# Kernel tuning notes

Measured on AMD Instinct MI355X. Metric: run time of the kernel, lower is better.

The kernel has to match this reference:

```python
import jax, jax.numpy as jnp
import numpy as np

QLEN, MLEN, BSZ = 1024, 1024, 2
D_MODEL, H, D_HEAD, D_FF = 1024, 16, 64, 4096
KLEN = QLEN + MLEN


def _ln(x, g, b, eps=1e-5):
    mu = jnp.mean(x, axis=-1, keepdims=True)
    var = jnp.var(x, axis=-1, keepdims=True)
    return (x - mu) * jax.lax.rsqrt(var + eps) * g + b


def _rel_shift(x):
    # x: [q, k, b, n] -> Transformer-XL relative shift
    q, k, b, n = x.shape
    zp = jnp.zeros((q, 1, b, n), x.dtype)
    xp = jnp.concatenate([zp, x], axis=1).reshape(k + 1, q, b, n)[1:]
    return xp.reshape(q, k, b, n)


def setup_inputs() -> dict:
    key = jax.random.key(0)
    ks = jax.random.split(key, 12)
    s = 0.02
    inp = {
        "input_": jax.random.normal(ks[0], (QLEN, BSZ, D_MODEL), jnp.float32),
        "mems": jax.random.normal(ks[1], (MLEN, BSZ, D_MODEL), jnp.float32),
        "pos_emb": jax.random.normal(ks[2], (KLEN, 1, D_MODEL), jnp.float32),
        # True = masked. Causal with memory: query i sees keys j <= i + MLEN
        "mask_tgt": jnp.triu(jnp.ones((QLEN, KLEN), bool), k=MLEN + 1),
        "ln1_g": jnp.ones((D_MODEL,), jnp.float32),
        "ln1_b": jnp.zeros((D_MODEL,), jnp.float32),
        "qkv_w": jax.random.normal(ks[3], (D_MODEL, 3 * H * D_HEAD), jnp.float32) * s,
        "qkv_b": jnp.zeros((3 * H * D_HEAD,), jnp.float32),
        "r_w": jax.random.normal(ks[4], (D_MODEL, H * D_HEAD), jnp.float32) * s,
        "r_w_bias": jax.random.normal(ks[5], (H, D_HEAD), jnp.float32) * s,
        "r_r_bias": jax.random.normal(ks[6], (H, D_HEAD), jnp.float32) * s,
        "o_w": jax.random.normal(ks[7], (H * D_HEAD, D_MODEL), jnp.float32) * s,
        "ln2_g": jnp.ones((D_MODEL,), jnp.float32),
        "ln2_b": jnp.zeros((D_MODEL,), jnp.float32),
        "ff_w1": jax.random.normal(ks[8], (D_MODEL, D_FF), jnp.float32) * s,
        "ff_b1": jnp.zeros((D_FF,), jnp.float32),
        "ff_w2": jax.random.normal(ks[9], (D_FF, D_MODEL), jnp.float32) * s,
        "ff_b2": jnp.zeros((D_MODEL,), jnp.float32),
    }
    return inp


def reference(input_, mems, pos_emb, mask_tgt, ln1_g, ln1_b, qkv_w, qkv_b,
              r_w, r_w_bias, r_r_bias, o_w, ln2_g, ln2_b,
              ff_w1, ff_b1, ff_w2, ff_b2):
    qlen, bsz, _ = input_.shape
    # --- pre-norm (applied to both current input and mems) ---
    q_in = _ln(input_, ln1_g, ln1_b)
    m_in = _ln(mems, ln1_g, ln1_b)
    cat = jnp.concatenate([m_in, q_in], axis=0)            # [klen, b, d]
    klen = cat.shape[0]
    heads = cat @ qkv_w + qkv_b                            # [klen, b, 3*h*dh]
    w_q, w_k, w_v = jnp.split(heads, 3, axis=-1)
    w_q = w_q[-qlen:].reshape(qlen, bsz, H, D_HEAD)        # [q, b, h, dh]
    w_k = w_k.reshape(klen, bsz, H, D_HEAD)
    w_v = w_v.reshape(klen, bsz, H, D_HEAD)
    r_k = (pos_emb[:, 0] @ r_w).reshape(klen, H, D_HEAD)   # [k, h, dh]

    AC = jnp.einsum('ibnd,jbnd->ijbn', w_q + r_w_bias, w_k)
    BD = jnp.einsum('ibnd,jnd->ijbn', w_q + r_r_bias, r_k)
    BD = _rel_shift(BD)
    scale = 1.0 / np.sqrt(D_HEAD)
    score = (AC + BD) * scale                              # [q, k, b, h]
    score = jnp.where(mask_tgt[:, :, None, None], -1e30, score)
    prob = jax.nn.softmax(score, axis=1)
    attn = jnp.einsum('ijbn,jbnd->ibnd', prob, w_v).reshape(qlen, bsz, H * D_HEAD)
    attn_out = attn @ o_w                                  # [q, b, d]
    x = input_ + attn_out                                  # residual (dropout = eval)

    # --- FFN block ---
    y = _ln(x, ln2_g, ln2_b)
    y = jax.nn.relu(y @ ff_w1 + ff_b1) @ ff_w2 + ff_b2
    return x + y
```

## Files before the change

kernel.cpp:

```cpp
#include <hip/hip_runtime.h>


typedef unsigned short u16;
typedef unsigned int   u32;
typedef __attribute__((ext_vector_type(8))) short bf16x8;
typedef __attribute__((ext_vector_type(4))) float f32x4;

struct alignas(16) U128 { u32 x[4]; };
struct alignas(16) F128 { float f[4]; };
struct alignas(8)  U64  { u32 x[2]; };

#define DEV static __device__ __forceinline__
#define MF(a, b, c) __builtin_amdgcn_mfma_f32_16x16x32_bf16((a), (b), (c), 0, 0, 0)

typedef __attribute__((address_space(1))) u32 as1_u32;
typedef __attribute__((address_space(3))) u32 as3_u32;
DEV void gload16(const void* g, void* l) {
  __builtin_amdgcn_global_load_lds((as1_u32*)g, (as3_u32*)l, 16, 0, 0);
}

DEV u16 f2bf(float f) {
  union { float f; u32 u; } v; v.f = f;
  u32 r = v.u + 0x7fffu + ((v.u >> 16) & 1u);
  return (u16)(r >> 16);
}
DEV float bf2f(u16 h) {
  union { u32 u; float f; } v; v.u = ((u32)h) << 16;
  return v.f;
}

template <int TWO>
__global__ __launch_bounds__(256) void ln_rows(
    const float* __restrict__ src, const float* __restrict__ src2,
    const float* __restrict__ g, const float* __restrict__ b,
    u16* __restrict__ dst)
{
  int row = blockIdx.x, tid = threadIdx.x;
  const float* s_;
  if constexpr (TWO) s_ = (row < 2048) ? src + (size_t)row * 1024
                                       : src2 + (size_t)(row - 2048) * 1024;
  else s_ = src + (size_t)row * 1024;
  F128 v = ((const F128*)s_)[tid];
  float s = v.f[0] + v.f[1] + v.f[2] + v.f[3];
  float q = v.f[0]*v.f[0] + v.f[1]*v.f[1] + v.f[2]*v.f[2] + v.f[3]*v.f[3];
#pragma unroll
  for (int off = 1; off < 64; off <<= 1) {
    s += __shfl_xor(s, off); q += __shfl_xor(q, off);
  }
  __shared__ float sh[8];
  int wid = tid >> 6;
  if ((tid & 63) == 0) { sh[wid] = s; sh[4 + wid] = q; }
  __syncthreads();
  s = sh[0] + sh[1] + sh[2] + sh[3];
  q = sh[4] + sh[5] + sh[6] + sh[7];
  float mu = s * (1.0f / 1024.0f);
  float rs = rsqrtf(q * (1.0f / 1024.0f) - mu * mu + 1e-5f);
  F128 g4 = ((const F128*)g)[tid];
  F128 b4 = ((const F128*)b)[tid];
  union { u16 h[4]; U64 u; } o;
#pragma unroll
  for (int j = 0; j < 4; j++)
    o.h[j] = f2bf((v.f[j] - mu) * rs * g4.f[j] + b4.f[j]);
  *(U64*)(dst + (size_t)row * 1024 + tid * 4) = o.u;
}

__global__ __launch_bounds__(256) void ln_fuse(
    const u16* __restrict__ p0, const u16* __restrict__ p1,
    const u16* __restrict__ p2, const u16* __restrict__ p3,
    const float* __restrict__ resid, const float* __restrict__ g,
    const float* __restrict__ b, float* __restrict__ X, u16* __restrict__ YN)
{
  int row = blockIdx.x, tid = threadIdx.x;
  U64 a = ((const U64*)(p0 + (size_t)row * 1024))[tid];
  U64 c = ((const U64*)(p1 + (size_t)row * 1024))[tid];
  U64 d = ((const U64*)(p2 + (size_t)row * 1024))[tid];
  U64 e = ((const U64*)(p3 + (size_t)row * 1024))[tid];
  F128 rv = ((const F128*)(resid + (size_t)row * 1024))[tid];
  float x[4];
#pragma unroll
  for (int k = 0; k < 2; k++) {
    x[2*k]   = bf2f((u16)a.x[k]) + bf2f((u16)c.x[k]) + bf2f((u16)d.x[k]) + bf2f((u16)e.x[k]) + rv.f[2*k];
    x[2*k+1] = bf2f((u16)(a.x[k] >> 16)) + bf2f((u16)(c.x[k] >> 16)) + bf2f((u16)(d.x[k] >> 16)) + bf2f((u16)(e.x[k] >> 16)) + rv.f[2*k+1];
  }
  F128 xo;
#pragma unroll
  for (int j = 0; j < 4; j++) xo.f[j] = x[j];
  *(F128*)(X + (size_t)row * 1024 + tid * 4) = xo;

  float s = x[0] + x[1] + x[2] + x[3];
  float q = x[0]*x[0] + x[1]*x[1] + x[2]*x[2] + x[3]*x[3];
#pragma unroll
  for (int off = 1; off < 64; off <<= 1) {
    s += __shfl_xor(s, off); q += __shfl_xor(q, off);
  }
  __shared__ float sh[8];
  int wid = tid >> 6;
  if ((tid & 63) == 0) { sh[wid] = s; sh[4 + wid] = q; }
  __syncthreads();
  s = sh[0] + sh[1] + sh[2] + sh[3];
  q = sh[4] + sh[5] + sh[6] + sh[7];
  float mu = s * (1.0f / 1024.0f);
  float rs = rsqrtf(q * (1.0f / 1024.0f) - mu * mu + 1e-5f);
  F128 g4 = ((const F128*)g)[tid];
  F128 b4 = ((const F128*)b)[tid];
  union { u16 h[4]; U64 u; } o;
#pragma unroll
  for (int j = 0; j < 4; j++)
    o.h[j] = f2bf((x[j] - mu) * rs * g4.f[j] + b4.f[j]);
  *(U64*)(YN + (size_t)row * 1024 + tid * 4) = o.u;
}

__global__ __launch_bounds__(256) void prep_weights(
    const float* __restrict__ qkvw, const float* __restrict__ rw,
    const float* __restrict__ oww, const float* __restrict__ fw1,
    const float* __restrict__ fw2, const float* __restrict__ pos,
    u16* __restrict__ WT_QKV, u16* __restrict__ WT_R, u16* __restrict__ WT_O,
    u16* __restrict__ WT_F1, u16* __restrict__ WT_F2, u16* __restrict__ POSB)
{
  int id = blockIdx.x, tid = threadIdx.x;
  if (id >= 3328) {
    int i = (id - 3328) * 256 + tid;
    F128 v = ((const F128*)pos)[i];
    union { u16 h[4]; U64 u; } o;
#pragma unroll
    for (int j = 0; j < 4; j++) o.h[j] = f2bf(v.f[j]);
    ((U64*)POSB)[i] = o.u;
    return;
  }
  const float* W; u16* Wt; int K, N, rem;
  if (id < 768)       { W = qkvw; Wt = WT_QKV; K = 1024; N = 3072; rem = id; }
  else if (id < 1024) { W = rw;   Wt = WT_R;   K = 1024; N = 1024; rem = id - 768; }
  else if (id < 1280) { W = oww;  Wt = WT_O;   K = 1024; N = 1024; rem = id - 1024; }
  else if (id < 2304) { W = fw1;  Wt = WT_F1;  K = 1024; N = 4096; rem = id - 1280; }
  else                { W = fw2;  Wt = WT_F2;  K = 4096; N = 1024; rem = id - 2304; }
  int nn = N >> 6;
  int k0 = (rem / nn) * 64, n0 = (rem % nn) * 64;
  __shared__ float t[64][65];
  int r = tid >> 6, c = tid & 63;
#pragma unroll
  for (int i = 0; i < 16; i++)
    t[r + i * 4][c] = W[(size_t)(k0 + r + i * 4) * N + n0 + c];
  __syncthreads();
#pragma unroll
  for (int i = 0; i < 16; i++) {
    int n = r + i * 4;
    Wt[(size_t)(n0 + n) * K + k0 + c] = f2bf(t[c][n]);
  }
}

template <int EPI, int NSPLIT>
__global__ __launch_bounds__(256, 2) void gemm_bt(
    const u16* __restrict__ A, const u16* __restrict__ Bt,
    u16* __restrict__ outb, const float* __restrict__ bias,
    u16* __restrict__ p0, u16* __restrict__ p1,
    u16* __restrict__ p2, u16* __restrict__ p3,
    int M, int N, int K)
{
  __shared__ u16 As[2][128 * 64];
  __shared__ u16 Bs[2][128 * 64];
  int tid = threadIdx.x;
  int m0 = blockIdx.x * 128, n0 = blockIdx.y * 128;
  int lane = tid & 63, wid = tid >> 6;
  int wr = wid >> 1, wc = wid & 1;
  f32x4 acc[4][4] = {};

  const int Kc = K / NSPLIT;
  const int kbase = (NSPLIT > 1) ? (int)blockIdx.z * Kc : 0;

  const int lrow = wid * 8 + (lane >> 3);
  const int lcol = (lane & 7) * 8;
  const u16* Ag = A  + (size_t)(m0 + lrow) * K + kbase + lcol;
  const u16* Bg = Bt + (size_t)(n0 + lrow) * K + kbase + lcol;

  auto stage = [&](int buf, int k0) {
#pragma unroll
    for (int i = 0; i < 4; i++) {
      gload16(Ag + (size_t)i * 32 * K + k0, &As[buf][(i * 4 + wid) * 512]);
      gload16(Bg + (size_t)i * 32 * K + k0, &Bs[buf][(i * 4 + wid) * 512]);
    }
  };

  stage(0, 0);
  __syncthreads();
  int cur = 0;
  for (int k0 = 0; k0 < Kc; k0 += 64) {
    if (k0 + 64 < Kc) stage(cur ^ 1, k0 + 64);
    bf16x8 af[2][4], bfr[2][4];
#pragma unroll
    for (int kc = 0; kc < 2; kc++)
#pragma unroll
      for (int f = 0; f < 4; f++) {
        af[kc][f]  = *(const bf16x8*)&As[cur][(wr * 64 + f * 16 + (lane & 15)) * 64 + kc * 32 + (lane >> 4) * 8];
        bfr[kc][f] = *(const bf16x8*)&Bs[cur][(wc * 64 + f * 16 + (lane & 15)) * 64 + kc * 32 + (lane >> 4) * 8];
      }
    __builtin_amdgcn_s_setprio(1);
#pragma unroll
    for (int kc = 0; kc < 2; kc++)
#pragma unroll
      for (int fi = 0; fi < 4; fi++)
#pragma unroll
        for (int fj = 0; fj < 4; fj++)
          acc[fi][fj] = MF(af[kc][fi], bfr[kc][fj], acc[fi][fj]);
    __builtin_amdgcn_s_setprio(0);
    __syncthreads();
    cur ^= 1;
  }

  u16* part = nullptr;
  if constexpr (NSPLIT > 1) {
    part = (blockIdx.z == 0) ? p0 : (blockIdx.z == 1) ? p1
         : (blockIdx.z == 2) ? p2 : p3;
  }
#pragma unroll
  for (int fi = 0; fi < 4; fi++)
#pragma unroll
    for (int fj = 0; fj < 4; fj++) {
      int col = n0 + wc * 64 + fj * 16 + (lane & 15);
      float bvv = (NSPLIT == 1 && bias != nullptr) ? bias[col] : 0.0f;
#pragma unroll
      for (int r = 0; r < 4; r++) {
        int row = m0 + wr * 64 + fi * 16 + (lane >> 4) * 4 + r;
        float v = acc[fi][fj][r] + bvv;
        if constexpr (NSPLIT > 1) {
          part[(size_t)row * N + col] = f2bf(v);
        } else {
          if constexpr (EPI == 1) v = fmaxf(v, 0.0f);
          outb[(size_t)row * N + col] = f2bf(v);
        }
      }
    }
}

template <int NS, int EPI>
__global__ __launch_bounds__(256) void reduce_splitb(
    const u16* __restrict__ p0, const u16* __restrict__ p1,
    const u16* __restrict__ p2, const u16* __restrict__ p3,
    const float* __restrict__ bias, const float* __restrict__ resid,
    u16* __restrict__ outb, float* __restrict__ outf, int N)
{
  int e = (blockIdx.x * 256 + threadIdx.x) * 8;
  U128 a = *(const U128*)(p0 + e);
  U128 c = *(const U128*)(p1 + e);
  float v[8];
#pragma unroll
  for (int k = 0; k < 4; k++) {
    v[2*k]   = bf2f((u16)a.x[k]) + bf2f((u16)c.x[k]);
    v[2*k+1] = bf2f((u16)(a.x[k] >> 16)) + bf2f((u16)(c.x[k] >> 16));
  }
  if constexpr (NS == 4) {
    U128 d2 = *(const U128*)(p2 + e);
    U128 d3 = *(const U128*)(p3 + e);
#pragma unroll
    for (int k = 0; k < 4; k++) {
      v[2*k]   += bf2f((u16)d2.x[k]) + bf2f((u16)d3.x[k]);
      v[2*k+1] += bf2f((u16)(d2.x[k] >> 16)) + bf2f((u16)(d3.x[k] >> 16));
    }
  }
  if constexpr (EPI == 2) {
    F128 r0 = *(const F128*)(resid + e);
    F128 r1 = *(const F128*)(resid + e + 4);
    int col = e % N;
    F128 o0, o1;
#pragma unroll
    for (int j = 0; j < 4; j++) {
      float b0 = (bias != nullptr) ? bias[col + j] : 0.0f;
      float b1 = (bias != nullptr) ? bias[col + 4 + j] : 0.0f;
      o0.f[j] = v[j] + b0 + r0.f[j];
      o1.f[j] = v[4 + j] + b1 + r1.f[j];
    }
    *(F128*)(outf + e) = o0;
    *(F128*)(outf + e + 4) = o1;
  } else {
    U128 o;
#pragma unroll
    for (int k = 0; k < 4; k++)
      o.x[k] = (u32)f2bf(v[2*k]) | ((u32)f2bf(v[2*k+1]) << 16);
    *(U128*)(outb + e) = o;
  }
}

__global__ __launch_bounds__(256) void extract_vt(
    const u16* __restrict__ heads, u16* __restrict__ Vt)
{
  __shared__ u16 t[64][72];
  int jt = blockIdx.x;
  int bh = blockIdx.y;
  int b = bh >> 4, h = bh & 15;
  int tid = threadIdx.x;
  int row = tid >> 2;
  int cc = (tid & 3) * 16;
#pragma unroll
  for (int i = 0; i < 2; i++)
    *(U128*)&t[row][cc + i * 8] =
        *(const U128*)&heads[(size_t)((jt * 64 + row) * 2 + b) * 3072 + 2048 + h * 64 + cc + i * 8];
  __syncthreads();
  int jc = tid & 63, dr = tid >> 6;
#pragma unroll
  for (int i = 0; i < 16; i++) {
    int d = dr + i * 4;
    Vt[((size_t)bh * 64 + d) * 2048 + jt * 64 + jc] = t[jc][d];
  }
}

__global__ __launch_bounds__(256, 2) void attn_fwd(
    const u16* __restrict__ heads, const u16* __restrict__ rk,
    const u16* __restrict__ Vt, const float* __restrict__ rwb,
    const float* __restrict__ rrb, u16* __restrict__ attnout)
{
  __shared__ u16 lds[37376];

  int tid = threadIdx.x, lane = tid & 63, wid = tid >> 6;
  int bh = blockIdx.x;
  int y = (int)blockIdx.y;
  int xt = (y < 8) ? y : 23 - y;
  int i0 = xt * 64;
  int b = bh >> 4, h = bh & 15;
  const float SCL = 0.18033688f;

  u16* Ps = lds + 32768;
  u16* Qw = lds;
  u16* Qr = lds + 4608;

  for (int c = tid; c < 512; c += 256) {
    int row = c >> 3, c8 = (c & 7) * 8;
    union { U128 v; u16 h[8]; } in, ow, orr;
    in.v = *(const U128*)&heads[(size_t)((1024 + i0 + row) * 2 + b) * 3072 + h * 64 + c8];
#pragma unroll
    for (int j = 0; j < 8; j++) {
      float q = bf2f(in.h[j]);
      ow.h[j]  = f2bf(q + rwb[h * 64 + c8 + j]);
      orr.h[j] = f2bf(q + rrb[h * 64 + c8 + j]);
    }
    *(U128*)&Qw[row * 72 + c8] = ow.v;
    *(U128*)&Qr[row * 72 + c8] = orr.v;
  }
  __syncthreads();

  bf16x8 qwf[2], qrf[2];
  int qrow = wid * 16 + (lane & 15);
#pragma unroll
  for (int kc = 0; kc < 2; kc++) {
    qwf[kc] = *(const bf16x8*)&Qw[qrow * 72 + kc * 32 + (lane >> 4) * 8];
    qrf[kc] = *(const bf16x8*)&Qr[qrow * 72 + kc * 32 + (lane >> 4) * 8];
  }
  __syncthreads();

  const int srow = lane >> 3;
  const int scol = 8 * ((lane & 7) ^ srow);

  auto stage = [&](int buf, int t) {
    int j0 = t * 64;
    u16* base = lds + buf * 16384;
#pragma unroll
    for (int i = 0; i < 2; i++) {
      int g8 = wid * 2 + i;
      int jr = j0 + g8 * 8 + srow;
      gload16(heads + (size_t)(jr * 2 + b) * 3072 + 1024 + h * 64 + scol,
              base + g8 * 512);
    }
#pragma unroll
    for (int i = 0; i < 2; i++) {
      int g8 = wid * 2 + i;
      int dr = g8 * 8 + srow;
      gload16(Vt + ((size_t)bh * 64 + dr) * 2048 + j0 + scol,
              base + 4096 + g8 * 512);
    }
    int rbase = 960 + j0 - i0;
#pragma unroll
    for (int i = 0; i < 4; i++) {
      int g8 = wid * 4 + i;
      int rr = rbase + g8 * 8 + srow;
      rr = rr < 0 ? 0 : (rr > 2047 ? 2047 : rr);
      gload16(rk + (size_t)rr * 1024 + h * 64 + scol,
              base + 8192 + g8 * 512);
    }
  };

  stage(0, 0);
  __syncthreads();

  float mrow[4], plrow[4];
  f32x4 o[4] = {};
  f32x4 bd[5];
#pragma unroll
  for (int r = 0; r < 4; r++) { mrow[r] = -1e30f; plrow[r] = 0.0f; }

  int nt = i0 / 64 + 17;
  const int roffw = 48 - wid * 16;
  const int g = lane >> 4, cc = lane & 15;
  const int rswz = 8 * (lane & 7);

  for (int t = 0; t < nt; t++) {
    const u16* base = lds + (t & 1) * 16384;
    if (t + 1 < nt) stage((t + 1) & 1, t + 1);

    const u16* Kb = base;
    const u16* Vb = base + 4096;
    const u16* Rb = base + 8192;

    f32x4 sAC[4] = {};
    if (t == 0) bd[0] = (f32x4){0.f, 0.f, 0.f, 0.f};
#pragma unroll
    for (int fb = 1; fb < 5; fb++) bd[fb] = (f32x4){0.f, 0.f, 0.f, 0.f};
    __builtin_amdgcn_s_setprio(1);
#pragma unroll
    for (int kc = 0; kc < 2; kc++) {
      int cb = (kc * 32 + g * 8) ^ rswz;
#pragma unroll
      for (int fj = 0; fj < 4; fj++) {
        bf16x8 kf = *(const bf16x8*)&Kb[(fj * 16 + (lane & 15)) * 64 + cb];
        sAC[fj] = MF(qwf[kc], kf, sAC[fj]);
      }
      if (t == 0) {
        bf16x8 rf = *(const bf16x8*)&Rb[(roffw + (lane & 15)) * 64 + cb];
        bd[0] = MF(qrf[kc], rf, bd[0]);
      }
#pragma unroll
      for (int fb = 1; fb < 5; fb++) {
        bf16x8 rf = *(const bf16x8*)&Rb[(roffw + fb * 16 + (lane & 15)) * 64 + cb];
        bd[fb] = MF(qrf[kc], rf, bd[fb]);
      }
    }
    __builtin_amdgcn_s_setprio(0);

    float p[4][4];
#pragma unroll
    for (int fj = 0; fj < 4; fj++)
#pragma unroll
      for (int r = 0; r < 4; r++) {
        int sh_ = 15 - 4 * g - r;
        int src = (lane & 48) | ((lane + sh_) & 15);
        float lo = __shfl(bd[fj][r], src);
        float hi = __shfl(bd[fj + 1][r], src);
        float bdv = (cc + sh_ < 16) ? lo : hi;
        p[fj][r] = (sAC[fj][r] + bdv) * SCL;
      }
    bd[0] = bd[4];

    if (t == nt - 1) {
#pragma unroll
      for (int fj = 0; fj < 4; fj++)
#pragma unroll
        for (int r = 0; r < 4; r++)
          if (fj * 16 + cc > 16 * wid + 4 * g + r) p[fj][r] = -1e30f;
    }

    float tmax[4];
#pragma unroll
    for (int r = 0; r < 4; r++)
      tmax[r] = fmaxf(fmaxf(p[0][r], p[1][r]), fmaxf(p[2][r], p[3][r]));

    bool ok = true;
#pragma unroll
    for (int r = 0; r < 4; r++) ok &= (tmax[r] <= mrow[r] + 12.0f);
    if (!__all(ok)) {
#pragma unroll
      for (int off = 1; off < 16; off <<= 1)
#pragma unroll
        for (int r = 0; r < 4; r++)
          tmax[r] = fmaxf(tmax[r], __shfl_xor(tmax[r], off));
#pragma unroll
      for (int r = 0; r < 4; r++) {
        float mn = fmaxf(mrow[r], tmax[r]);
        float ms = exp2f(mrow[r] - mn);
        mrow[r] = mn;
        plrow[r] *= ms;
#pragma unroll
        for (int fd = 0; fd < 4; fd++) o[fd][r] *= ms;
      }
    }

#pragma unroll
    for (int fj = 0; fj < 4; fj++)
#pragma unroll
      for (int r = 0; r < 4; r++) {
        float e = exp2f(p[fj][r] - mrow[r]);
        plrow[r] += e;
        Ps[(wid * 16 + (lane >> 4) * 4 + r) * 72 + fj * 16 + (lane & 15)] = f2bf(e);
      }
    __builtin_amdgcn_s_setprio(1);
#pragma unroll
    for (int kc = 0; kc < 2; kc++) {
      bf16x8 pf = *(const bf16x8*)&Ps[(wid * 16 + (lane & 15)) * 72 + kc * 32 + g * 8];
      int cb = (kc * 32 + g * 8) ^ rswz;
#pragma unroll
      for (int fd = 0; fd < 4; fd++) {
        bf16x8 vf = *(const bf16x8*)&Vb[(fd * 16 + (lane & 15)) * 64 + cb];
        o[fd] = MF(pf, vf, o[fd]);
      }
    }
    __builtin_amdgcn_s_setprio(0);

    __syncthreads();
  }

#pragma unroll
  for (int off = 1; off < 16; off <<= 1)
#pragma unroll
    for (int r = 0; r < 4; r++)
      plrow[r] += __shfl_xor(plrow[r], off);
#pragma unroll
  for (int fd = 0; fd < 4; fd++)
#pragma unroll
    for (int r = 0; r < 4; r++) {
      int ii2 = (lane >> 4) * 4 + r;
      int row = (i0 + wid * 16 + ii2) * 2 + b;
      attnout[(size_t)row * 1024 + h * 64 + fd * 16 + (lane & 15)] = f2bf(o[fd][r] / plrow[r]);
    }
}

extern "C" void kernel_launch(void* const* d_in, const int* in_sizes, int n_in,
                              void* d_out, int out_size, void* d_ws, size_t ws_size,
                              hipStream_t stream)
{
  const float* input_ = (const float*)d_in[0];
  const float* mems   = (const float*)d_in[1];
  const float* pos    = (const float*)d_in[2];
  const float* ln1g = (const float*)d_in[4];
  const float* ln1b = (const float*)d_in[5];
  const float* qkvw = (const float*)d_in[6];
  const float* qkvb = (const float*)d_in[7];
  const float* rw   = (const float*)d_in[8];
  const float* rwb  = (const float*)d_in[9];
  const float* rrb  = (const float*)d_in[10];
  const float* ow   = (const float*)d_in[11];
  const float* ln2g = (const float*)d_in[12];
  const float* ln2b = (const float*)d_in[13];
  const float* fw1  = (const float*)d_in[14];
  const float* fb1  = (const float*)d_in[15];
  const float* fw2  = (const float*)d_in[16];
  const float* fb2  = (const float*)d_in[17];
  float* out = (float*)d_out;

  char* w = (char*)d_ws;
  u16* WT_QKV = (u16*)(w + 0);
  u16* WT_R   = (u16*)(w + 6291456);
  u16* WT_O   = (u16*)(w + 8388608);
  u16* WT_F1  = (u16*)(w + 10485760);
  u16* WT_F2  = (u16*)(w + 18874368);
  u16* POSB   = (u16*)(w + 27262976);
  u16* ATTN   = POSB;
  u16* CATLN  = (u16*)(w + 31457280);
  u16* HEADS  = (u16*)(w + 39845888);
  u16* H1     = HEADS;
  float* X    = (float*)(w + 56623104);
  u16* RK     = (u16*)(w + 65011712);
  u16* VT     = (u16*)(w + 69206016);
  u16* YN     = VT;

  u16* RKP0 = (u16*)(w + 31457280);
  u16* RKP1 = (u16*)(w + 35651584);
  u16* RKP2 = (u16*)(w + 69206016);
  u16* RKP3 = (u16*)(w + 73400320);
  u16* OWP0 = (u16*)(w + 39845888);
  u16* OWP1 = (u16*)(w + 44040192);
  u16* OWP2 = (u16*)(w + 48234496);
  u16* OWP3 = (u16*)(w + 52428800);
  u16* F2P0 = (u16*)(w + 0);
  u16* F2P1 = (u16*)(w + 10485760);
  u16* F2P2 = (u16*)(w + 31457280);
  u16* F2P3 = (u16*)(w + 65011712);

  dim3 blk(256);

  prep_weights<<<dim3(5376), blk, 0, stream>>>(
      qkvw, rw, ow, fw1, fw2, pos, WT_QKV, WT_R, WT_O, WT_F1, WT_F2, POSB);

  ln_rows<1><<<dim3(4096), blk, 0, stream>>>(mems, input_, ln1g, ln1b, CATLN);

  gemm_bt<0, 1><<<dim3(32, 24), blk, 0, stream>>>(
      CATLN, WT_QKV, HEADS, qkvb, nullptr, nullptr, nullptr, nullptr, 4096, 3072, 1024);
  gemm_bt<0, 4><<<dim3(16, 8, 4), blk, 0, stream>>>(
      POSB, WT_R, nullptr, nullptr, RKP0, RKP1, RKP2, RKP3, 2048, 1024, 1024);
  reduce_splitb<4, 0><<<dim3(1024), blk, 0, stream>>>(
      RKP0, RKP1, RKP2, RKP3, nullptr, nullptr, RK, nullptr, 1024);

  extract_vt<<<dim3(32, 32), blk, 0, stream>>>(HEADS, VT);
  attn_fwd<<<dim3(32, 16), blk, 0, stream>>>(HEADS, RK, VT, rwb, rrb, ATTN);

  gemm_bt<0, 4><<<dim3(16, 8, 4), blk, 0, stream>>>(
      ATTN, WT_O, nullptr, nullptr, OWP0, OWP1, OWP2, OWP3, 2048, 1024, 1024);
  ln_fuse<<<dim3(2048), blk, 0, stream>>>(
      OWP0, OWP1, OWP2, OWP3, input_, ln2g, ln2b, X, YN);

  gemm_bt<1, 1><<<dim3(16, 32), blk, 0, stream>>>(
      YN, WT_F1, H1, fb1, nullptr, nullptr, nullptr, nullptr, 2048, 4096, 1024);
  gemm_bt<0, 4><<<dim3(16, 8, 4), blk, 0, stream>>>(
      H1, WT_F2, nullptr, nullptr, F2P0, F2P1, F2P2, F2P3, 2048, 1024, 4096);
  reduce_splitb<4, 2><<<dim3(1024), blk, 0, stream>>>(
      F2P0, F2P1, F2P2, F2P3, fb2, X, nullptr, out, 1024);
}
```

Baseline: 223.3 us.

## Fuse LN1 into prep kernel and single-buffer GEMM LDS for higher occupancy

Merges the first layernorm launch into the weight-prep kernel as extra blocks, removing one kernel launch. Separately, the GEMM drops LDS double-buffering, halving shared memory, and raises launch bounds to 4 blocks per CU so latency is hidden by occupancy rather than prefetch. This costs the overlap of global loads with MFMA inside each block, and the higher launch-bounds target may squeeze registers for the 64-float accumulator.

```diff
diff --git a/kernel.cpp b/kernel.cpp
--- a/kernel.cpp
+++ b/kernel.cpp
@@ -29,20 +29,31 @@
   return v.f;
 }
 
-template <int TWO>
-__global__ __launch_bounds__(256) void ln_rows(
-    const float* __restrict__ src, const float* __restrict__ src2,
-    const float* __restrict__ g, const float* __restrict__ b,
-    u16* __restrict__ dst)
+__global__ __launch_bounds__(256) void ln_fuse(
+    const u16* __restrict__ p0, const u16* __restrict__ p1,
+    const u16* __restrict__ p2, const u16* __restrict__ p3,
+    const float* __restrict__ resid, const float* __restrict__ g,
+    const float* __restrict__ b, float* __restrict__ X, u16* __restrict__ YN)
 {
   int row = blockIdx.x, tid = threadIdx.x;
-  const float* s_;
-  if constexpr (TWO) s_ = (row < 2048) ? src + (size_t)row * 1024
-                                       : src2 + (size_t)(row - 2048) * 1024;
-  else s_ = src + (size_t)row * 1024;
-  F128 v = ((const F128*)s_)[tid];
-  float s = v.f[0] + v.f[1] + v.f[2] + v.f[3];
-  float q = v.f[0]*v.f[0] + v.f[1]*v.f[1] + v.f[2]*v.f[2] + v.f[3]*v.f[3];
+  U64 a = ((const U64*)(p0 + (size_t)row * 1024))[tid];
+  U64 c = ((const U64*)(p1 + (size_t)row * 1024))[tid];
+  U64 d = ((const U64*)(p2 + (size_t)row * 1024))[tid];
+  U64 e = ((const U64*)(p3 + (size_t)row * 1024))[tid];
+  F128 rv = ((const F128*)(resid + (size_t)row * 1024))[tid];
+  float x[4];
+#pragma unroll
+  for (int k = 0; k < 2; k++) {
+    x[2*k]   = bf2f((u16)a.x[k]) + bf2f((u16)c.x[k]) + bf2f((u16)d.x[k]) + bf2f((u16)e.x[k]) + rv.f[2*k];
+    x[2*k+1] = bf2f((u16)(a.x[k] >> 16)) + bf2f((u16)(c.x[k] >> 16)) + bf2f((u16)(d.x[k] >> 16)) + bf2f((u16)(e.x[k] >> 16)) + rv.f[2*k+1];
+  }
+  F128 xo;
+#pragma unroll
+  for (int j = 0; j < 4; j++) xo.f[j] = x[j];
+  *(F128*)(X + (size_t)row * 1024 + tid * 4) = xo;
+
+  float s = x[0] + x[1] + x[2] + x[3];
+  float q = x[0]*x[0] + x[1]*x[1] + x[2]*x[2] + x[3]*x[3];
 #pragma unroll
   for (int off = 1; off < 64; off <<= 1) {
     s += __shfl_xor(s, off); q += __shfl_xor(q, off);
@@ -60,52 +71,6 @@
   union { u16 h[4]; U64 u; } o;
 #pragma unroll
   for (int j = 0; j < 4; j++)
-    o.h[j] = f2bf((v.f[j] - mu) * rs * g4.f[j] + b4.f[j]);
-  *(U64*)(dst + (size_t)row * 1024 + tid * 4) = o.u;
-}
-
-__global__ __launch_bounds__(256) void ln_fuse(
-    const u16* __restrict__ p0, const u16* __restrict__ p1,
-    const u16* __restrict__ p2, const u16* __restrict__ p3,
-    const float* __restrict__ resid, const float* __restrict__ g,
-    const float* __restrict__ b, float* __restrict__ X, u16* __restrict__ YN)
-{
-  int row = blockIdx.x, tid = threadIdx.x;
-  U64 a = ((const U64*)(p0 + (size_t)row * 1024))[tid];
-  U64 c = ((const U64*)(p1 + (size_t)row * 1024))[tid];
-  U64 d = ((const U64*)(p2 + (size_t)row * 1024))[tid];
-  U64 e = ((const U64*)(p3 + (size_t)row * 1024))[tid];
-  F128 rv = ((const F128*)(resid + (size_t)row * 1024))[tid];
-  float x[4];
-#pragma unroll
-  for (int k = 0; k < 2; k++) {
-    x[2*k]   = bf2f((u16)a.x[k]) + bf2f((u16)c.x[k]) + bf2f((u16)d.x[k]) + bf2f((u16)e.x[k]) + rv.f[2*k];
-    x[2*k+1] = bf2f((u16)(a.x[k] >> 16)) + bf2f((u16)(c.x[k] >> 16)) + bf2f((u16)(d.x[k] >> 16)) + bf2f((u16)(e.x[k] >> 16)) + rv.f[2*k+1];
-  }
-  F128 xo;
-#pragma unroll
-  for (int j = 0; j < 4; j++) xo.f[j] = x[j];
-  *(F128*)(X + (size_t)row * 1024 + tid * 4) = xo;
-
-  float s = x[0] + x[1] + x[2] + x[3];
-  float q = x[0]*x[0] + x[1]*x[1] + x[2]*x[2] + x[3]*x[3];
-#pragma unroll
-  for (int off = 1; off < 64; off <<= 1) {
-    s += __shfl_xor(s, off); q += __shfl_xor(q, off);
-  }
-  __shared__ float sh[8];
-  int wid = tid >> 6;
-  if ((tid & 63) == 0) { sh[wid] = s; sh[4 + wid] = q; }
-  __syncthreads();
-  s = sh[0] + sh[1] + sh[2] + sh[3];
-  q = sh[4] + sh[5] + sh[6] + sh[7];
-  float mu = s * (1.0f / 1024.0f);
-  float rs = rsqrtf(q * (1.0f / 1024.0f) - mu * mu + 1e-5f);
-  F128 g4 = ((const F128*)g)[tid];
-  F128 b4 = ((const F128*)b)[tid];
-  union { u16 h[4]; U64 u; } o;
-#pragma unroll
-  for (int j = 0; j < 4; j++)
     o.h[j] = f2bf((x[j] - mu) * rs * g4.f[j] + b4.f[j]);
   *(U64*)(YN + (size_t)row * 1024 + tid * 4) = o.u;
 }
@@ -114,10 +79,41 @@
     const float* __restrict__ qkvw, const float* __restrict__ rw,
     const float* __restrict__ oww, const float* __restrict__ fw1,
     const float* __restrict__ fw2, const float* __restrict__ pos,
+    const float* __restrict__ mems, const float* __restrict__ input_,
+    const float* __restrict__ ln1g, const float* __restrict__ ln1b,
     u16* __restrict__ WT_QKV, u16* __restrict__ WT_R, u16* __restrict__ WT_O,
-    u16* __restrict__ WT_F1, u16* __restrict__ WT_F2, u16* __restrict__ POSB)
+    u16* __restrict__ WT_F1, u16* __restrict__ WT_F2, u16* __restrict__ POSB,
+    u16* __restrict__ CATLN)
 {
   int id = blockIdx.x, tid = threadIdx.x;
+  if (id >= 5376) {
+    int row = id - 5376;
+    const float* s_ = (row < 2048) ? mems + (size_t)row * 1024
+                                   : input_ + (size_t)(row - 2048) * 1024;
+    F128 v = ((const F128*)s_)[tid];
+    float s = v.f[0] + v.f[1] + v.f[2] + v.f[3];
+    float q = v.f[0]*v.f[0] + v.f[1]*v.f[1] + v.f[2]*v.f[2] + v.f[3]*v.f[3];
+#pragma unroll
+    for (int off = 1; off < 64; off <<= 1) {
+      s += __shfl_xor(s, off); q += __shfl_xor(q, off);
+    }
+    __shared__ float sh[8];
+    int wid = tid >> 6;
+    if ((tid & 63) == 0) { sh[wid] = s; sh[4 + wid] = q; }
+    __syncthreads();
+    s = sh[0] + sh[1] + sh[2] + sh[3];
+    q = sh[4] + sh[5] + sh[6] + sh[7];
+    float mu = s * (1.0f / 1024.0f);
+    float rs = rsqrtf(q * (1.0f / 1024.0f) - mu * mu + 1e-5f);
+    F128 g4 = ((const F128*)ln1g)[tid];
+    F128 b4 = ((const F128*)ln1b)[tid];
+    union { u16 h[4]; U64 u; } o;
+#pragma unroll
+    for (int j = 0; j < 4; j++)
+      o.h[j] = f2bf((v.f[j] - mu) * rs * g4.f[j] + b4.f[j]);
+    *(U64*)(CATLN + (size_t)row * 1024 + tid * 4) = o.u;
+    return;
+  }
   if (id >= 3328) {
     int i = (id - 3328) * 256 + tid;
     F128 v = ((const F128*)pos)[i];
@@ -149,15 +145,15 @@
 }
 
 template <int EPI, int NSPLIT>
-__global__ __launch_bounds__(256, 2) void gemm_bt(
+__global__ __launch_bounds__(256, 4) void gemm_bt(
     const u16* __restrict__ A, const u16* __restrict__ Bt,
     u16* __restrict__ outb, const float* __restrict__ bias,
     u16* __restrict__ p0, u16* __restrict__ p1,
     u16* __restrict__ p2, u16* __restrict__ p3,
     int M, int N, int K)
 {
-  __shared__ u16 As[2][128 * 64];
-  __shared__ u16 Bs[2][128 * 64];
+  __shared__ u16 As[128 * 64];
+  __shared__ u16 Bs[128 * 64];
   int tid = threadIdx.x;
   int m0 = blockIdx.x * 128, n0 = blockIdx.y * 128;
   int lane = tid & 63, wid = tid >> 6;
@@ -172,26 +168,20 @@
   const u16* Ag = A  + (size_t)(m0 + lrow) * K + kbase + lcol;
   const u16* Bg = Bt + (size_t)(n0 + lrow) * K + kbase + lcol;
 
-  auto stage = [&](int buf, int k0) {
+  for (int k0 = 0; k0 < Kc; k0 += 64) {
 #pragma unroll
     for (int i = 0; i < 4; i++) {
-      gload16(Ag + (size_t)i * 32 * K + k0, &As[buf][(i * 4 + wid) * 512]);
-      gload16(Bg + (size_t)i * 32 * K + k0, &Bs[buf][(i * 4 + wid) * 512]);
-    }
-  };
-
-  stage(0, 0);
-  __syncthreads();
-  int cur = 0;
-  for (int k0 = 0; k0 < Kc; k0 += 64) {
-    if (k0 + 64 < Kc) stage(cur ^ 1, k0 + 64);
+      gload16(Ag + (size_t)i * 32 * K + k0, &As[(i * 4 + wid) * 512]);
+      gload16(Bg + (size_t)i * 32 * K + k0, &Bs[(i * 4 + wid) * 512]);
+    }
+    __syncthreads();
     bf16x8 af[2][4], bfr[2][4];
 #pragma unroll
     for (int kc = 0; kc < 2; kc++)
 #pragma unroll
       for (int f = 0; f < 4; f++) {
-        af[kc][f]  = *(const bf16x8*)&As[cur][(wr * 64 + f * 16 + (lane & 15)) * 64 + kc * 32 + (lane >> 4) * 8];
-        bfr[kc][f] = *(const bf16x8*)&Bs[cur][(wc * 64 + f * 16 + (lane & 15)) * 64 + kc * 32 + (lane >> 4) * 8];
+        af[kc][f]  = *(const bf16x8*)&As[(wr * 64 + f * 16 + (lane & 15)) * 64 + kc * 32 + (lane >> 4) * 8];
+        bfr[kc][f] = *(const bf16x8*)&Bs[(wc * 64 + f * 16 + (lane & 15)) * 64 + kc * 32 + (lane >> 4) * 8];
       }
     __builtin_amdgcn_s_setprio(1);
 #pragma unroll
@@ -203,7 +193,6 @@
           acc[fi][fj] = MF(af[kc][fi], bfr[kc][fj], acc[fi][fj]);
     __builtin_amdgcn_s_setprio(0);
     __syncthreads();
-    cur ^= 1;
   }
 
   u16* part = nullptr;
@@ -563,10 +552,9 @@
 
   dim3 blk(256);
 
-  prep_weights<<<dim3(5376), blk, 0, stream>>>(
-      qkvw, rw, ow, fw1, fw2, pos, WT_QKV, WT_R, WT_O, WT_F1, WT_F2, POSB);
-
-  ln_rows<1><<<dim3(4096), blk, 0, stream>>>(mems, input_, ln1g, ln1b, CATLN);
+  prep_weights<<<dim3(9472), blk, 0, stream>>>(
+      qkvw, rw, ow, fw1, fw2, pos, mems, input_, ln1g, ln1b,
+      WT_QKV, WT_R, WT_O, WT_F1, WT_F2, POSB, CATLN);
 
   gemm_bt<0, 1><<<dim3(32, 24), blk, 0, stream>>>(
       CATLN, WT_QKV, HEADS, qkvb, nullptr, nullptr, nullptr, nullptr, 4096, 3072, 1024);
```

Result: slower. 350.0 us (+56.7%).
